# Kernel tuning notes

Hardware: AMD Instinct MI355X
Metric: run time of the kernel (lower is better)

## Reference

```python
import jax, jax.numpy as jnp
import numpy as np

H, D, HID, DIN = 2, 32, 64, 128
NQ, NA, NK = 100000, 200000, 200000
E_KQ, E_QK, E_QA, E_AQ = 800000, 800000, 400000, 400000
EP, EN = 100000, 100000


def setup_inputs() -> dict:
    key = jax.random.key(0)
    ks = jax.random.split(key, 32)
    f = lambda i, shape, s=0.05: jax.random.normal(ks[i], shape, dtype=jnp.float32) * s
    ri = lambda i, n, hi: jax.random.randint(ks[i], (n,), 0, hi)
    return {
        'xq': f(0, (NQ, DIN), 1.0), 'xa': f(1, (NA, DIN), 1.0), 'xk': f(2, (NK, DIN), 1.0),
        'lin_w': f(3, (3, DIN, HID)), 'lin_b': f(4, (3, HID)),
        'k_w': f(5, (3, HID, HID)), 'k_b': f(6, (3, HID)),
        'q_w': f(7, (3, HID, HID)), 'q_b': f(8, (3, HID)),
        'v_w': f(9, (3, HID, HID)), 'v_b': f(10, (3, HID)),
        'a_w': f(11, (3, HID, HID)), 'a_b': f(12, (3, HID)),
        'a_rel': f(13, (4, H, D, D), 0.2), 'm_rel': f(14, (4, H, D, D), 0.2),
        'p_rel': jnp.ones((4, H), dtype=jnp.float32),  # PyG init: ones
        'skip': jnp.ones((3,), dtype=jnp.float32),     # PyG init: ones
        'ei_kq_src': ri(15, E_KQ, NK), 'ei_kq_dst': ri(16, E_KQ, NQ),
        'ei_qk_src': ri(17, E_QK, NQ), 'ei_qk_dst': ri(18, E_QK, NA * 0 + NK),
        'ei_qa_src': ri(19, E_QA, NQ), 'ei_qa_dst': ri(20, E_QA, NA),
        'ei_aq_src': ri(21, E_AQ, NA), 'ei_aq_dst': ri(22, E_AQ, NQ),
        'pos_src': ri(23, EP, NQ), 'pos_dst': ri(24, EP, NA),
        'neg_src': ri(25, EN, NQ), 'neg_dst': ri(26, EN, NA),
    }


def _seg_softmax(alpha, dst, n):
    # softmax over incoming edges per destination node (per head)
    m = jax.ops.segment_max(alpha, dst, num_segments=n)
    m = jnp.where(jnp.isfinite(m), m, 0.0)
    e = jnp.exp(alpha - m[dst])
    s = jax.ops.segment_sum(e, dst, num_segments=n)
    return e / (s[dst] + 1e-16)


def hgt_forward(xq, xa, xk, lin_w, lin_b, k_w, k_b, q_w, q_b, v_w, v_b, a_w, a_b,
                a_rel, m_rel, p_rel, skip, edges):
    # node types: 0=question, 1=answer, 2=knowledge
    xs = [jax.nn.relu(x @ lin_w[i] + lin_b[i]) for i, x in enumerate([xq, xa, xk])]
    ns = [x.shape[0] for x in xs]
    k = [(x @ k_w[i] + k_b[i]).reshape(-1, H, D) for i, x in enumerate(xs)]
    q = [(x @ q_w[i] + q_b[i]).reshape(-1, H, D) for i, x in enumerate(xs)]
    v = [(x @ v_w[i] + v_b[i]).reshape(-1, H, D) for i, x in enumerate(xs)]
    out = [jnp.zeros((n, H, D), dtype=xs[0].dtype) for n in ns]
    scale = 1.0 / jnp.sqrt(jnp.float32(D))
    for st, dt, r, es, ed in edges:
        # per-edge-type head-wise key/value transforms (applied at node level)
        k_rel = jnp.einsum('nhd,hde->nhe', k[st], a_rel[r])
        v_rel = jnp.einsum('nhd,hde->nhe', v[st], m_rel[r])
        alpha = (q[dt][ed] * k_rel[es]).sum(-1) * p_rel[r] * scale  # [E,H]
        a = _seg_softmax(alpha, ed, ns[dt])
        msg = a[:, :, None] * v_rel[es]  # [E,H,D]
        out[dt] = out[dt] + jax.ops.segment_sum(msg, ed, num_segments=ns[dt])
    z = []
    for i in range(3):
        o = jax.nn.gelu(out[i].reshape(-1, H * D), approximate=False) @ a_w[i] + a_b[i]
        beta = jax.nn.sigmoid(skip[i])
        z.append(beta * o + (1.0 - beta) * xs[i])
    return z  # [z_question, z_answer, z_knowledge]; note: HGT.forward never applies self.lin


def reference(xq, xa, xk, lin_w, lin_b, k_w, k_b, q_w, q_b, v_w, v_b, a_w, a_b,
              a_rel, m_rel, p_rel, skip,
              ei_kq_src, ei_kq_dst, ei_qk_src, ei_qk_dst, ei_qa_src, ei_qa_dst,
              ei_aq_src, ei_aq_dst, pos_src, pos_dst, neg_src, neg_dst):
    edges = [
        (2, 0, 0, ei_kq_src, ei_kq_dst),  # knowledge -> question
        (0, 2, 1, ei_qk_src, ei_qk_dst),  # question -> knowledge
        (0, 1, 2, ei_qa_src, ei_qa_dst),  # question -> answer
        (1, 0, 3, ei_aq_src, ei_aq_dst),  # answer -> question
    ]
    zq, za, zk = hgt_forward(xq, xa, xk, lin_w, lin_b, k_w, k_b, q_w, q_b, v_w, v_b,
                             a_w, a_b, a_rel, m_rel, p_rel, skip, edges)
    pos_pred = jax.nn.sigmoid((zq[pos_src] * za[pos_dst]).sum(-1))
    neg_pred = jax.nn.sigmoid((zq[neg_src] * za[neg_dst]).sum(-1))
    return (pos_pred, neg_pred, zq, za, zk)
```

## Files before the change

kernel.cpp:

```cpp
#include <hip/hip_runtime.h>
#include <math.h>

namespace {

constexpr int NQn = 100000, NAn = 200000, NKn = 200000;
constexpr int EPc = 100000, ENc = 100000;
constexpr int ETOT = 2400000, NSEG = 600000;

constexpr long XSB_OFF  = 0;
constexpr long OUTB_OFF = 16000000;
constexpr long QBF_OFF  = 32000000;
constexpr long KV_OFF   = 48000000;
constexpr long ZB_OFF   = 86500000;
constexpr long WTB_OFF  = 96200000;
constexpr long WFB_OFF  = 96250000;
constexpr long INT_OFF  = 96300000;
constexpr long DEG_I  = 0;
constexpr long CUR_I  = 600000;
constexpr long OFFS_I = 1200000;
constexpr long PART_I = 1800064;
constexpr long CSRC_I = 1801088;

constexpr int LINT_U = 0;
constexpr int QT_U   = 24576;
constexpr int AT_U   = 36864;
constexpr int WFT_U  = 49152;

__constant__ long c_rbase[4] = {0, 200000, 300032, 400064};

typedef __attribute__((ext_vector_type(8))) short bf16x8;
typedef __attribute__((ext_vector_type(4))) float f32x4;

__device__ inline f32x4 mfma16(bf16x8 a, bf16x8 b, f32x4 c) {
    return __builtin_amdgcn_mfma_f32_16x16x32_bf16(a, b, c, 0, 0, 0);
}

__device__ inline float gelu_f(float x) {
    return 0.5f * x * (1.0f + erff(x * 0.7071067811865475f));
}
__device__ inline float bf2f(unsigned short u) {
    return __uint_as_float(((unsigned)u) << 16);
}
__device__ inline unsigned short f2bf(float f) {
    unsigned u = __float_as_uint(f);
    return (unsigned short)((u + 0x7fffu + ((u >> 16) & 1u)) >> 16);
}

__device__ inline void type_of_block128(int b, int& t, int& n0) {
    if (b < 782)       { t = 0; n0 = b * 128; }
    else if (b < 2345) { t = 1; n0 = (b - 782) * 128; }
    else               { t = 2; n0 = (b - 2345) * 128; }
}

template<int K>
__device__ inline void stage_bf16(unsigned short* lds, const unsigned short* src,
                                  int n0, int n, int tid)
{
    constexpr int CPR = K / 8;
    for (int c = tid; c < 128 * CPR; c += 256) {
        int row = c / CPR, kc = c % CPR;
        int node = n0 + row; if (node > n - 1) node = n - 1;
        uint4 v = *(const uint4*)&src[(long)node * K + kc * 8];
        int byte = (row * K + kc * 8) * 2;
        *(uint4*)((char*)lds + (byte ^ ((row & 7) << 4))) = v;
    }
}

__device__ inline void stage_out_gelu(unsigned short* lds, const unsigned short* src,
                                      int n0, int n, int tid)
{
    for (int c = tid; c < 128 * 8; c += 256) {
        int row = c >> 3, kc = c & 7;
        int node = n0 + row; if (node > n - 1) node = n - 1;
        uint4 v = *(const uint4*)&src[(long)node * 64 + kc * 8];
        float f0 = gelu_f(bf2f((unsigned short)(v.x & 0xffffu)));
        float f1 = gelu_f(bf2f((unsigned short)(v.x >> 16)));
        float f2 = gelu_f(bf2f((unsigned short)(v.y & 0xffffu)));
        float f3 = gelu_f(bf2f((unsigned short)(v.y >> 16)));
        float f4 = gelu_f(bf2f((unsigned short)(v.z & 0xffffu)));
        float f5 = gelu_f(bf2f((unsigned short)(v.z >> 16)));
        float f6 = gelu_f(bf2f((unsigned short)(v.w & 0xffffu)));
        float f7 = gelu_f(bf2f((unsigned short)(v.w >> 16)));
        uint4 o;
        o.x = (unsigned)f2bf(f0) | ((unsigned)f2bf(f1) << 16);
        o.y = (unsigned)f2bf(f2) | ((unsigned)f2bf(f3) << 16);
        o.z = (unsigned)f2bf(f4) | ((unsigned)f2bf(f5) << 16);
        o.w = (unsigned)f2bf(f6) | ((unsigned)f2bf(f7) << 16);
        int byte = (row * 64 + kc * 8) * 2;
        *(uint4*)((char*)lds + (byte ^ ((row & 7) << 4))) = o;
    }
}

template<int K>
__device__ inline void stage_f32(unsigned short* lds, const float* src,
                                 int n0, int n, int tid)
{
    constexpr int CPR = K / 8;
    for (int c = tid; c < 128 * CPR; c += 256) {
        int row = c / CPR, kc = c % CPR;
        int node = n0 + row; if (node > n - 1) node = n - 1;
        const float* sp = &src[(long)node * K + kc * 8];
        float4 f0 = *(const float4*)sp, f1 = *(const float4*)(sp + 4);
        uint4 v;
        v.x = (unsigned)f2bf(f0.x) | ((unsigned)f2bf(f0.y) << 16);
        v.y = (unsigned)f2bf(f0.z) | ((unsigned)f2bf(f0.w) << 16);
        v.z = (unsigned)f2bf(f1.x) | ((unsigned)f2bf(f1.y) << 16);
        v.w = (unsigned)f2bf(f1.z) | ((unsigned)f2bf(f1.w) << 16);
        int byte = (row * K + kc * 8) * 2;
        *(uint4*)((char*)lds + (byte ^ ((row & 7) << 4))) = v;
    }
}

template<int N, int K>
__device__ inline void stage_w(unsigned short* lds, const unsigned short* wt, int tid)
{
    constexpr int CPR = K / 8;
    for (int c = tid; c < N * CPR; c += 256) {
        int nr = c / CPR, kc = c % CPR;
        uint4 v = *(const uint4*)&wt[nr * K + kc * 8];
        int byte = (nr * K + kc * 8) * 2;
        *(uint4*)((char*)lds + (byte ^ ((nr & 7) << 4))) = v;
    }
}

template<int K, int NF>
__device__ inline void mfma_coreT(const unsigned short* ldsX, const unsigned short* ldsW,
                                  f32x4 (&acc)[2][NF], int lane, int w)
{
    const int lrow = lane & 15, lk = (lane >> 4) * 8;
    #pragma unroll
    for (int ks = 0; ks < K / 32; ++ks) {
        bf16x8 a[2], b[NF];
        #pragma unroll
        for (int mf = 0; mf < 2; ++mf) {
            int row = w * 32 + mf * 16 + lrow;
            int byte = (row * K + ks * 32 + lk) * 2;
            a[mf] = *(const bf16x8*)((const char*)ldsX + (byte ^ ((row & 7) << 4)));
        }
        #pragma unroll
        for (int nf = 0; nf < NF; ++nf) {
            int nr = nf * 16 + lrow;
            int byte = (nr * K + ks * 32 + lk) * 2;
            b[nf] = *(const bf16x8*)((const char*)ldsW + (byte ^ ((nr & 7) << 4)));
        }
        #pragma unroll
        for (int mf = 0; mf < 2; ++mf)
            #pragma unroll
            for (int nf = 0; nf < NF; ++nf)
                acc[mf][nf] = mfma16(b[nf], a[mf], acc[mf][nf]);
    }
}

__global__ void prep_w(const float* __restrict__ lin_w, const float* __restrict__ q_w,
                       const float* __restrict__ a_w, unsigned short* __restrict__ wtb)
{
    int i = blockIdx.x * 256 + threadIdx.x;
    if (i < 24576) {
        int t = i / 8192, rem = i % 8192, nn = rem >> 7, kk = rem & 127;
        wtb[LINT_U + i] = f2bf(lin_w[t * 8192 + kk * 64 + nn]);
    } else if (i < 36864) {
        int j = i - 24576;
        int t = j / 4096, rem = j % 4096, nn = rem >> 6, kk = rem & 63;
        wtb[QT_U + j] = f2bf(q_w[t * 4096 + kk * 64 + nn]);
    } else if (i < 49152) {
        int j = i - 36864;
        int t = j / 4096, rem = j % 4096, nn = rem >> 6, kk = rem & 63;
        wtb[AT_U + j] = f2bf(a_w[t * 4096 + kk * 64 + nn]);
    }
}

__global__ void fuse_weights(const float* __restrict__ kw, const float* __restrict__ kb,
                             const float* __restrict__ vw, const float* __restrict__ vb,
                             const float* __restrict__ a_rel, const float* __restrict__ m_rel,
                             unsigned short* __restrict__ wtb, float* __restrict__ wfb)
{
    const int r = blockIdx.x;
    const int st_tab[4] = {2, 0, 0, 1};
    const int st = st_tab[r];
    const int tid = threadIdx.x;
    for (int idx = tid; idx < 8192; idx += 256) {
        int d = idx >> 7, c = idx & 127;
        int i = c >> 1, which = c & 1;
        int h = i >> 5, e = i & 31;
        const float* w   = (which ? vw : kw) + st * 4096;
        const float* rel = (which ? m_rel : a_rel) + r * 2048;
        float s = 0.f;
        #pragma unroll
        for (int c32 = 0; c32 < 32; ++c32)
            s += w[d * 64 + h * 32 + c32] * rel[h * 1024 + c32 * 32 + e];
        wtb[WFT_U + r * 8192 + c * 64 + d] = f2bf(s);
    }
    for (int idx = tid; idx < 128; idx += 256) {
        int i = idx >> 1, which = idx & 1;
        int h = i >> 5, e = i & 31;
        const float* b   = (which ? vb : kb) + st * 64;
        const float* rel = (which ? m_rel : a_rel) + r * 2048;
        float s = 0.f;
        #pragma unroll
        for (int c32 = 0; c32 < 32; ++c32)
            s += b[h * 32 + c32] * rel[h * 1024 + c32 * 32 + e];
        wfb[r * 128 + idx] = s;
    }
}

__global__ void __launch_bounds__(256)
lin_mfma(const float* __restrict__ xq, const float* __restrict__ xa,
         const float* __restrict__ xk, const unsigned short* __restrict__ wtb,
         const float* __restrict__ lin_b, unsigned short* __restrict__ xsb)
{
    __shared__ unsigned short ldsX[128 * 128];
    __shared__ unsigned short ldsW[64 * 128];
    int t, n0; type_of_block128(blockIdx.x, t, n0);
    const int cnt[3] = {NQn, NAn, NKn};
    const long noff[3] = {0, NQn, NQn + NAn};
    const float* X = (t == 0) ? xq : (t == 1) ? xa : xk;
    const int n = cnt[t];
    const int tid = threadIdx.x;

    stage_w<64, 128>(ldsW, wtb + LINT_U + t * 8192, tid);
    stage_f32<128>(ldsX, X, n0, n, tid);
    __syncthreads();

    const int w = tid >> 6, lane = tid & 63;
    f32x4 acc[2][4] = {};
    mfma_coreT<128, 4>(ldsX, ldsW, acc, lane, w);

    const int nodeL = lane & 15, colG = (lane >> 4) * 4;
    #pragma unroll
    for (int mf = 0; mf < 2; ++mf) {
        int node = n0 + w * 32 + mf * 16 + nodeL;
        if (node < n) {
            #pragma unroll
            for (int nf = 0; nf < 4; ++nf) {
                int col0 = nf * 16 + colG;
                float4 bv = *(const float4*)&lin_b[t * 64 + col0];
                ushort4 o;
                o.x = f2bf(fmaxf(acc[mf][nf][0] + bv.x, 0.f));
                o.y = f2bf(fmaxf(acc[mf][nf][1] + bv.y, 0.f));
                o.z = f2bf(fmaxf(acc[mf][nf][2] + bv.z, 0.f));
                o.w = f2bf(fmaxf(acc[mf][nf][3] + bv.w, 0.f));
                *(ushort4*)&xsb[(noff[t] + node) * 64 + col0] = o;
            }
        }
    }
}

__global__ void __launch_bounds__(256)
qkv_mfma(const unsigned short* __restrict__ xsb, const unsigned short* __restrict__ wtb,
         const float* __restrict__ q_b, const float* __restrict__ wfb,
         unsigned short* __restrict__ qbf, unsigned short* __restrict__ kvb)
{
    __shared__ unsigned short ldsX[128 * 64];
    __shared__ unsigned short ldsW[128 * 64];
    int t, n0; type_of_block128(blockIdx.x, t, n0);
    const int cnt[3] = {NQn, NAn, NKn};
    const long noff[3] = {0, NQn, NQn + NAn};
    const int n = cnt[t];
    const int tid = threadIdx.x;
    const int relA_tab[3] = {1, 3, 0};
    const int rA = relA_tab[t];
    const int nrel = (t == 0) ? 2 : 1;

    stage_bf16<64>(ldsX, xsb + noff[t] * 64, n0, n, tid);
    stage_w<64, 64>(ldsW, wtb + QT_U + t * 4096, tid);
    __syncthreads();

    const int w = tid >> 6, lane = tid & 63;
    const int nodeL = lane & 15, colG = (lane >> 4) * 4;

    {
        f32x4 acc[2][4] = {};
        mfma_coreT<64, 4>(ldsX, ldsW, acc, lane, w);
        #pragma unroll
        for (int mf = 0; mf < 2; ++mf) {
            int node = n0 + w * 32 + mf * 16 + nodeL;
            if (node < n) {
                #pragma unroll
                for (int nf = 0; nf < 4; ++nf) {
                    int col0 = nf * 16 + colG;
                    float4 bv = *(const float4*)&q_b[t * 64 + col0];
                    ushort4 o;
                    o.x = f2bf(acc[mf][nf][0] + bv.x);
                    o.y = f2bf(acc[mf][nf][1] + bv.y);
                    o.z = f2bf(acc[mf][nf][2] + bv.z);
                    o.w = f2bf(acc[mf][nf][3] + bv.w);
                    *(ushort4*)&qbf[(noff[t] + node) * 64 + col0] = o;
                }
            }
        }
    }
    for (int ri = 0; ri < nrel; ++ri) {
        const int r = (ri == 0) ? rA : 2;
        const long rb = c_rbase[r];
        __syncthreads();
        stage_w<128, 64>(ldsW, wtb + WFT_U + r * 8192, tid);
        __syncthreads();
        f32x4 acc[2][8] = {};
        mfma_coreT<64, 8>(ldsX, ldsW, acc, lane, w);
        #pragma unroll
        for (int mf = 0; mf < 2; ++mf) {
            int node = n0 + w * 32 + mf * 16 + nodeL;
            if (node < n) {
                #pragma unroll
                for (int nf = 0; nf < 8; ++nf) {
                    int col0 = nf * 16 + colG;
                    float4 bv = *(const float4*)&wfb[r * 128 + col0];
                    ushort4 o;
                    o.x = f2bf(acc[mf][nf][0] + bv.x);
                    o.y = f2bf(acc[mf][nf][1] + bv.y);
                    o.z = f2bf(acc[mf][nf][2] + bv.z);
                    o.w = f2bf(acc[mf][nf][3] + bv.w);
                    *(ushort4*)&kvb[(rb + node) * 128 + col0] = o;
                }
            }
        }
    }
}

__global__ void __launch_bounds__(256)
head_mfma(const unsigned short* __restrict__ outb, const unsigned short* __restrict__ xsb,
          const unsigned short* __restrict__ wtb, const float* __restrict__ a_b,
          const float* __restrict__ skip, float* __restrict__ z,
          unsigned short* __restrict__ zb)
{
    __shared__ unsigned short ldsX[128 * 64];
    __shared__ unsigned short ldsW[64 * 64];
    int t, n0; type_of_block128(blockIdx.x, t, n0);
    const int cnt[3] = {NQn, NAn, NKn};
    const long noff[3] = {0, NQn, NQn + NAn};
    const long zoff[3] = {200000L, 6600000L, 19400000L};
    const int n = cnt[t];
    const int tid = threadIdx.x;

    stage_w<64, 64>(ldsW, wtb + AT_U + t * 4096, tid);
    stage_out_gelu(ldsX, outb + noff[t] * 64, n0, n, tid);
    __syncthreads();

    const int w = tid >> 6, lane = tid & 63;
    f32x4 acc[2][4] = {};
    mfma_coreT<64, 4>(ldsX, ldsW, acc, lane, w);

    const float beta = 1.f / (1.f + expf(-skip[t]));
    const int nodeL = lane & 15, colG = (lane >> 4) * 4;
    #pragma unroll
    for (int mf = 0; mf < 2; ++mf) {
        int node = n0 + w * 32 + mf * 16 + nodeL;
        if (node < n) {
            #pragma unroll
            for (int nf = 0; nf < 4; ++nf) {
                int col0 = nf * 16 + colG;
                float4 bv = *(const float4*)&a_b[t * 64 + col0];
                ushort4 rv = *(const ushort4*)&xsb[(noff[t] + node) * 64 + col0];
                float4 o;
                o.x = beta * (acc[mf][nf][0] + bv.x) + (1.f - beta) * bf2f(rv.x);
                o.y = beta * (acc[mf][nf][1] + bv.y) + (1.f - beta) * bf2f(rv.y);
                o.z = beta * (acc[mf][nf][2] + bv.z) + (1.f - beta) * bf2f(rv.z);
                o.w = beta * (acc[mf][nf][3] + bv.w) + (1.f - beta) * bf2f(rv.w);
                *(float4*)&z[zoff[t] + (long)node * 64 + col0] = o;
                if (t < 2) {
                    ushort4 p;
                    p.x = f2bf(o.x); p.y = f2bf(o.y); p.z = f2bf(o.z); p.w = f2bf(o.w);
                    long zrow = (t == 0) ? (long)node : 100000L + node;
                    *(ushort4*)&zb[zrow * 64 + col0] = p;
                }
            }
        }
    }
}

__global__ void csr_count_all(const int* __restrict__ d0, const int* __restrict__ d1,
                              const int* __restrict__ d2, const int* __restrict__ d3,
                              int* __restrict__ deg)
{
    int gid = blockIdx.x * 256 + threadIdx.x;
    if (gid < 800000)       atomicAdd(&deg[d0[gid]], 1);
    else if (gid < 1600000) atomicAdd(&deg[100000 + d1[gid - 800000]], 1);
    else if (gid < 2000000) atomicAdd(&deg[300000 + d2[gid - 1600000]], 1);
    else if (gid < 2400000) atomicAdd(&deg[500000 + d3[gid - 2000000]], 1);
}

__global__ void csr_fill_all(const int* __restrict__ s0, const int* __restrict__ d0,
                             const int* __restrict__ s1, const int* __restrict__ d1,
                             const int* __restrict__ s2, const int* __restrict__ d2,
                             const int* __restrict__ s3, const int* __restrict__ d3,
                             const int* __restrict__ off, int* __restrict__ cur,
                             int* __restrict__ csrc)
{
    int gid = blockIdx.x * 256 + threadIdx.x;
    int seg, s;
    if (gid < 800000)       { seg = d0[gid];                    s = s0[gid]; }
    else if (gid < 1600000) { seg = 100000 + d1[gid - 800000];  s = s1[gid - 800000]; }
    else if (gid < 2000000) { seg = 300000 + d2[gid - 1600000]; s = s2[gid - 1600000]; }
    else if (gid < 2400000) { seg = 500000 + d3[gid - 2000000]; s = s3[gid - 2000000]; }
    else return;
    int slot = off[seg] + atomicAdd(&cur[seg], 1);
    csrc[slot] = s;
}

__global__ void scan1(const int* __restrict__ in, int* __restrict__ out,
                      int* __restrict__ part, int n)
{
    __shared__ int lds[256];
    const int tid = threadIdx.x;
    const int base = blockIdx.x * 1024 + tid * 4;
    int v[4];
    #pragma unroll
    for (int k = 0; k < 4; ++k) v[k] = (base + k < n) ? in[base + k] : 0;
    int tsum = v[0] + v[1] + v[2] + v[3];
    lds[tid] = tsum;
    __syncthreads();
    for (int off = 1; off < 256; off <<= 1) {
        int t = (tid >= off) ? lds[tid - off] : 0;
        __syncthreads();
        lds[tid] += t;
        __syncthreads();
    }
    int excl = lds[tid] - tsum;
    #pragma unroll
    for (int k = 0; k < 4; ++k) {
        if (base + k < n) out[base + k] = excl;
        excl += v[k];
    }
    if (tid == 255) part[blockIdx.x] = lds[255];
}

__global__ void scan2(int* __restrict__ part, int nb)
{
    __shared__ int lds[256];
    const int tid = threadIdx.x;
    const int base = tid * 4;
    int v[4];
    #pragma unroll
    for (int k = 0; k < 4; ++k) v[k] = (base + k < nb) ? part[base + k] : 0;
    int tsum = v[0] + v[1] + v[2] + v[3];
    lds[tid] = tsum;
    __syncthreads();
    for (int off = 1; off < 256; off <<= 1) {
        int t = (tid >= off) ? lds[tid - off] : 0;
        __syncthreads();
        lds[tid] += t;
        __syncthreads();
    }
    int excl = lds[tid] - tsum;
    #pragma unroll
    for (int k = 0; k < 4; ++k) {
        if (base + k < nb) part[base + k] = excl;
        excl += v[k];
    }
}

__global__ void scan3(int* __restrict__ off, const int* __restrict__ part, int n, int E)
{
    int i = blockIdx.x * 256 + threadIdx.x;
    if (i < n) off[i] += part[i >> 10];
    if (i == 0) off[n] = E;
}

__device__ inline void attn_node(const int* __restrict__ csrc, int begin, int end,
                                 const unsigned short* __restrict__ kvt,
                                 const float qv[4], int j, float res[4])
{
    float ss = 0.f, a0 = 0.f, a1 = 0.f, a2 = 0.f, a3 = 0.f;

    for (int t = begin; t < end; t += 2) {
        bool vB = (t + 1 < end);
        int sA = csrc[t];
        int sB = csrc[vB ? t + 1 : t];
        uint4 kA = *(const uint4*)(kvt + (long)sA * 128 + j * 8);
        uint4 kB = *(const uint4*)(kvt + (long)sB * 128 + j * 8);

        float ka0 = __uint_as_float(kA.x << 16), va0 = __uint_as_float(kA.x & 0xffff0000u);
        float ka1 = __uint_as_float(kA.y << 16), va1 = __uint_as_float(kA.y & 0xffff0000u);
        float ka2 = __uint_as_float(kA.z << 16), va2 = __uint_as_float(kA.z & 0xffff0000u);
        float ka3 = __uint_as_float(kA.w << 16), va3 = __uint_as_float(kA.w & 0xffff0000u);
        float kb0 = __uint_as_float(kB.x << 16), vb0 = __uint_as_float(kB.x & 0xffff0000u);
        float kb1 = __uint_as_float(kB.y << 16), vb1 = __uint_as_float(kB.y & 0xffff0000u);
        float kb2 = __uint_as_float(kB.z << 16), vb2 = __uint_as_float(kB.z & 0xffff0000u);
        float kb3 = __uint_as_float(kB.w << 16), vb3 = __uint_as_float(kB.w & 0xffff0000u);

        float pA = ka0 * qv[0] + ka1 * qv[1] + ka2 * qv[2] + ka3 * qv[3];
        float pB = kb0 * qv[0] + kb1 * qv[1] + kb2 * qv[2] + kb3 * qv[3];
        pA += __shfl_xor(pA, 1);  pB += __shfl_xor(pB, 1);
        pA += __shfl_xor(pA, 2);  pB += __shfl_xor(pB, 2);
        pA += __shfl_xor(pA, 4);  pB += __shfl_xor(pB, 4);

        float wA = exp2f(fminf(pA, 115.f));
        float wB = vB ? exp2f(fminf(pB, 115.f)) : 0.f;

        ss += wA + wB;
        a0 += wA * va0 + wB * vb0;
        a1 += wA * va1 + wB * vb1;
        a2 += wA * va2 + wB * vb2;
        a3 += wA * va3 + wB * vb3;
    }

    float inv = 1.f / (ss + 1e-16f);
    res[0] = a0 * inv; res[1] = a1 * inv; res[2] = a2 * inv; res[3] = a3 * inv;
}

__global__ void __launch_bounds__(256)
attn_all(const int* __restrict__ off, const int* __restrict__ csrc,
         const unsigned short* __restrict__ qbf, const unsigned short* __restrict__ kv,
         const float* __restrict__ prel, float scale, unsigned short* __restrict__ outb)
{
    const int tid = threadIdx.x;
    const int nid = blockIdx.x * 16 + (tid >> 4);
    const int j = tid & 15;
    const int h = j >> 3;
    const float l2e = 1.4426950408889634f;

    long row; int segA, segB = -1; long kbA, kbB = 0; float psA, psB = 0.f;
    if (nid < 100000) {
        row = nid;
        segA = nid;            kbA = c_rbase[0]; psA = prel[0 + h] * scale * l2e;
        segB = 500000 + nid;   kbB = c_rbase[3]; psB = prel[6 + h] * scale * l2e;
    } else if (nid < 300000) {
        int kk = nid - 100000;
        row = 300000 + kk;
        segA = 100000 + kk;    kbA = c_rbase[1]; psA = prel[2 + h] * scale * l2e;
    } else {
        int aa = nid - 300000;
        row = 100000 + aa;
        segA = 300000 + aa;    kbA = c_rbase[2]; psA = prel[4 + h] * scale * l2e;
    }

    ushort4 q4 = *(const ushort4*)&qbf[row * 64 + 4 * j];
    float qraw[4] = {bf2f(q4.x), bf2f(q4.y), bf2f(q4.z), bf2f(q4.w)};

    float res[4];
    {
        float qv[4] = {qraw[0] * psA, qraw[1] * psA, qraw[2] * psA, qraw[3] * psA};
        attn_node(csrc, off[segA], off[segA + 1], kv + kbA * 128, qv, j, res);
    }
    if (segB >= 0) {
        float qv[4] = {qraw[0] * psB, qraw[1] * psB, qraw[2] * psB, qraw[3] * psB};
        float r2[4];
        attn_node(csrc, off[segB], off[segB + 1], kv + kbB * 128, qv, j, r2);
        res[0] += r2[0]; res[1] += r2[1]; res[2] += r2[2]; res[3] += r2[3];
    }

    ushort4 o;
    o.x = f2bf(res[0]); o.y = f2bf(res[1]); o.z = f2bf(res[2]); o.w = f2bf(res[3]);
    *(ushort4*)&outb[row * 64 + 4 * j] = o;
}

__global__ void pred_all(const int* __restrict__ psrc, const int* __restrict__ pdst,
                         const int* __restrict__ nsrc, const int* __restrict__ ndst,
                         const unsigned short* __restrict__ zb, float* __restrict__ out)
{
    int t = blockIdx.x * 256 + threadIdx.x;
    int g = t >> 3, lane = t & 7;
    if (g >= EPc + ENc) return;
    int s, d;
    if (g < EPc) { s = psrc[g]; d = pdst[g]; }
    else         { int gg = g - EPc; s = nsrc[gg]; d = ndst[gg]; }
    uint4 zs = *(const uint4*)&zb[(long)s * 64 + lane * 8];
    uint4 zd = *(const uint4*)&zb[(100000L + d) * 64 + lane * 8];
    float p = 0.f;
    p += bf2f((unsigned short)(zs.x & 0xffffu)) * bf2f((unsigned short)(zd.x & 0xffffu));
    p += bf2f((unsigned short)(zs.x >> 16))     * bf2f((unsigned short)(zd.x >> 16));
    p += bf2f((unsigned short)(zs.y & 0xffffu)) * bf2f((unsigned short)(zd.y & 0xffffu));
    p += bf2f((unsigned short)(zs.y >> 16))     * bf2f((unsigned short)(zd.y >> 16));
    p += bf2f((unsigned short)(zs.z & 0xffffu)) * bf2f((unsigned short)(zd.z & 0xffffu));
    p += bf2f((unsigned short)(zs.z >> 16))     * bf2f((unsigned short)(zd.z >> 16));
    p += bf2f((unsigned short)(zs.w & 0xffffu)) * bf2f((unsigned short)(zd.w & 0xffffu));
    p += bf2f((unsigned short)(zs.w >> 16))     * bf2f((unsigned short)(zd.w >> 16));
    p += __shfl_xor(p, 1);
    p += __shfl_xor(p, 2);
    p += __shfl_xor(p, 4);
    if (lane == 0) out[g] = 1.f / (1.f + expf(-p));
}

}

extern "C" void kernel_launch(void* const* d_in, const int* in_sizes, int n_in,
                              void* d_out, int out_size, void* d_ws, size_t ws_size,
                              hipStream_t stream)
{
    const float* xq    = (const float*)d_in[0];
    const float* xa    = (const float*)d_in[1];
    const float* xk    = (const float*)d_in[2];
    const float* lin_w = (const float*)d_in[3];
    const float* lin_b = (const float*)d_in[4];
    const float* k_w   = (const float*)d_in[5];
    const float* k_b   = (const float*)d_in[6];
    const float* q_w   = (const float*)d_in[7];
    const float* q_b   = (const float*)d_in[8];
    const float* v_w   = (const float*)d_in[9];
    const float* v_b   = (const float*)d_in[10];
    const float* a_w   = (const float*)d_in[11];
    const float* a_b   = (const float*)d_in[12];
    const float* a_rel = (const float*)d_in[13];
    const float* m_rel = (const float*)d_in[14];
    const float* p_rel = (const float*)d_in[15];
    const float* skip  = (const float*)d_in[16];
    const int* esrc[4] = {(const int*)d_in[17], (const int*)d_in[19], (const int*)d_in[21], (const int*)d_in[23]};
    const int* edst[4] = {(const int*)d_in[18], (const int*)d_in[20], (const int*)d_in[22], (const int*)d_in[24]};
    const int* pos_src = (const int*)d_in[25];
    const int* pos_dst = (const int*)d_in[26];
    const int* neg_src = (const int*)d_in[27];
    const int* neg_dst = (const int*)d_in[28];

    float* ws   = (float*)d_ws;
    float* outp = (float*)d_out;
    int*   wi   = (int*)(ws + INT_OFF);
    unsigned short* xsb  = (unsigned short*)(ws + XSB_OFF);
    unsigned short* outb = (unsigned short*)(ws + OUTB_OFF);
    unsigned short* qbf  = (unsigned short*)(ws + QBF_OFF);
    unsigned short* kvb  = (unsigned short*)(ws + KV_OFF);
    unsigned short* zbb  = (unsigned short*)(ws + ZB_OFF);
    unsigned short* wtb  = (unsigned short*)(ws + WTB_OFF);
    float*          wfb  = ws + WFB_OFF;

    hipMemsetAsync(wi + DEG_I, 0, 1200000L * sizeof(int), stream);
    csr_count_all<<<(ETOT + 255) / 256, 256, 0, stream>>>(
        edst[0], edst[1], edst[2], edst[3], wi + DEG_I);
    const int nb = (NSEG + 1023) / 1024;
    scan1<<<nb, 256, 0, stream>>>(wi + DEG_I, wi + OFFS_I, wi + PART_I, NSEG);
    scan2<<<1, 256, 0, stream>>>(wi + PART_I, nb);
    scan3<<<(NSEG + 255) / 256, 256, 0, stream>>>(wi + OFFS_I, wi + PART_I, NSEG, ETOT);
    csr_fill_all<<<(ETOT + 255) / 256, 256, 0, stream>>>(
        esrc[0], edst[0], esrc[1], edst[1], esrc[2], edst[2], esrc[3], edst[3],
        wi + OFFS_I, wi + CUR_I, wi + CSRC_I);

    fuse_weights<<<4, 256, 0, stream>>>(k_w, k_b, v_w, v_b, a_rel, m_rel, wtb, wfb);
    prep_w<<<192, 256, 0, stream>>>(lin_w, q_w, a_w, wtb);

    lin_mfma<<<3908, 256, 0, stream>>>(xq, xa, xk, wtb, lin_b, xsb);
    qkv_mfma<<<3908, 256, 0, stream>>>(xsb, wtb, q_b, wfb, qbf, kvb);

    const float scale = 0.17677669529663687f;
    attn_all<<<31250, 256, 0, stream>>>(wi + OFFS_I, wi + CSRC_I, qbf, kvb,
                                        p_rel, scale, outb);

    head_mfma<<<3908, 256, 0, stream>>>(outb, xsb, wtb, a_b, skip, outp, zbb);

    pred_all<<<(200000 * 8 + 255) / 256, 256, 0, stream>>>(
        pos_src, pos_dst, neg_src, neg_dst, zbb, outp);
}
```

Before: 653.1 us.

## Fuse input projection with QKV projection and merge weight prep kernels

The input linear+ReLU projection and the Q/K/V projection now run in one kernel. The projected features stay in LDS for the second GEMM instead of being re-read from global memory, though xsb is still written because the head stage needs it. The two weight-preparation kernels are merged into one launch. The attention inner loop now processes four edges per iteration instead of two to raise memory-level parallelism, at the cost of more registers.

Result: faster. 636.1 us (-2.6%).

```diff
diff --git a/kernel.cpp b/kernel.cpp
--- a/kernel.cpp
+++ b/kernel.cpp
@@ -50,20 +50,6 @@
     if (b < 782)       { t = 0; n0 = b * 128; }
     else if (b < 2345) { t = 1; n0 = (b - 782) * 128; }
     else               { t = 2; n0 = (b - 2345) * 128; }
-}
-
-template<int K>
-__device__ inline void stage_bf16(unsigned short* lds, const unsigned short* src,
-                                  int n0, int n, int tid)
-{
-    constexpr int CPR = K / 8;
-    for (int c = tid; c < 128 * CPR; c += 256) {
-        int row = c / CPR, kc = c % CPR;
-        int node = n0 + row; if (node > n - 1) node = n - 1;
-        uint4 v = *(const uint4*)&src[(long)node * K + kc * 8];
-        int byte = (row * K + kc * 8) * 2;
-        *(uint4*)((char*)lds + (byte ^ ((row & 7) << 4))) = v;
-    }
 }
 
 __device__ inline void stage_out_gelu(unsigned short* lds, const unsigned short* src,
@@ -151,126 +137,112 @@
     }
 }
 
-__global__ void prep_w(const float* __restrict__ lin_w, const float* __restrict__ q_w,
-                       const float* __restrict__ a_w, unsigned short* __restrict__ wtb)
-{
-    int i = blockIdx.x * 256 + threadIdx.x;
-    if (i < 24576) {
-        int t = i / 8192, rem = i % 8192, nn = rem >> 7, kk = rem & 127;
-        wtb[LINT_U + i] = f2bf(lin_w[t * 8192 + kk * 64 + nn]);
-    } else if (i < 36864) {
-        int j = i - 24576;
-        int t = j / 4096, rem = j % 4096, nn = rem >> 6, kk = rem & 63;
-        wtb[QT_U + j] = f2bf(q_w[t * 4096 + kk * 64 + nn]);
-    } else if (i < 49152) {
-        int j = i - 36864;
-        int t = j / 4096, rem = j % 4096, nn = rem >> 6, kk = rem & 63;
-        wtb[AT_U + j] = f2bf(a_w[t * 4096 + kk * 64 + nn]);
-    }
-}
-
-__global__ void fuse_weights(const float* __restrict__ kw, const float* __restrict__ kb,
-                             const float* __restrict__ vw, const float* __restrict__ vb,
-                             const float* __restrict__ a_rel, const float* __restrict__ m_rel,
-                             unsigned short* __restrict__ wtb, float* __restrict__ wfb)
-{
-    const int r = blockIdx.x;
-    const int st_tab[4] = {2, 0, 0, 1};
-    const int st = st_tab[r];
+__global__ void prep_all(const float* __restrict__ lin_w, const float* __restrict__ q_w,
+                         const float* __restrict__ a_w,
+                         const float* __restrict__ kw, const float* __restrict__ kb,
+                         const float* __restrict__ vw, const float* __restrict__ vb,
+                         const float* __restrict__ a_rel, const float* __restrict__ m_rel,
+                         unsigned short* __restrict__ wtb, float* __restrict__ wfb)
+{
     const int tid = threadIdx.x;
-    for (int idx = tid; idx < 8192; idx += 256) {
-        int d = idx >> 7, c = idx & 127;
-        int i = c >> 1, which = c & 1;
-        int h = i >> 5, e = i & 31;
-        const float* w   = (which ? vw : kw) + st * 4096;
-        const float* rel = (which ? m_rel : a_rel) + r * 2048;
-        float s = 0.f;
-        #pragma unroll
-        for (int c32 = 0; c32 < 32; ++c32)
-            s += w[d * 64 + h * 32 + c32] * rel[h * 1024 + c32 * 32 + e];
-        wtb[WFT_U + r * 8192 + c * 64 + d] = f2bf(s);
-    }
-    for (int idx = tid; idx < 128; idx += 256) {
-        int i = idx >> 1, which = idx & 1;
-        int h = i >> 5, e = i & 31;
-        const float* b   = (which ? vb : kb) + st * 64;
-        const float* rel = (which ? m_rel : a_rel) + r * 2048;
-        float s = 0.f;
-        #pragma unroll
-        for (int c32 = 0; c32 < 32; ++c32)
-            s += b[h * 32 + c32] * rel[h * 1024 + c32 * 32 + e];
-        wfb[r * 128 + idx] = s;
+    if (blockIdx.x < 4) {
+        const int r = blockIdx.x;
+        const int st_tab[4] = {2, 0, 0, 1};
+        const int st = st_tab[r];
+        for (int idx = tid; idx < 8192; idx += 256) {
+            int d = idx >> 7, c = idx & 127;
+            int i = c >> 1, which = c & 1;
+            int h = i >> 5, e = i & 31;
+            const float* w   = (which ? vw : kw) + st * 4096;
+            const float* rel = (which ? m_rel : a_rel) + r * 2048;
+            float s = 0.f;
+            #pragma unroll
+            for (int c32 = 0; c32 < 32; ++c32)
+                s += w[d * 64 + h * 32 + c32] * rel[h * 1024 + c32 * 32 + e];
+            wtb[WFT_U + r * 8192 + c * 64 + d] = f2bf(s);
+        }
+        for (int idx = tid; idx < 128; idx += 256) {
+            int i = idx >> 1, which = idx & 1;
+            int h = i >> 5, e = i & 31;
+            const float* b   = (which ? vb : kb) + st * 64;
+            const float* rel = (which ? m_rel : a_rel) + r * 2048;
+            float s = 0.f;
+            #pragma unroll
+            for (int c32 = 0; c32 < 32; ++c32)
+                s += b[h * 32 + c32] * rel[h * 1024 + c32 * 32 + e];
+            wfb[r * 128 + idx] = s;
+        }
+    } else {
+        int i = (blockIdx.x - 4) * 256 + tid;
+        if (i < 24576) {
+            int t = i / 8192, rem = i % 8192, nn = rem >> 7, kk = rem & 127;
+            wtb[LINT_U + i] = f2bf(lin_w[t * 8192 + kk * 64 + nn]);
+        } else if (i < 36864) {
+            int j = i - 24576;
+            int t = j / 4096, rem = j % 4096, nn = rem >> 6, kk = rem & 63;
+            wtb[QT_U + j] = f2bf(q_w[t * 4096 + kk * 64 + nn]);
+        } else if (i < 49152) {
+            int j = i - 36864;
+            int t = j / 4096, rem = j % 4096, nn = rem >> 6, kk = rem & 63;
+            wtb[AT_U + j] = f2bf(a_w[t * 4096 + kk * 64 + nn]);
+        }
     }
 }
 
 __global__ void __launch_bounds__(256)
-lin_mfma(const float* __restrict__ xq, const float* __restrict__ xa,
-         const float* __restrict__ xk, const unsigned short* __restrict__ wtb,
-         const float* __restrict__ lin_b, unsigned short* __restrict__ xsb)
+linqkv_mfma(const float* __restrict__ xq, const float* __restrict__ xa,
+            const float* __restrict__ xk, const unsigned short* __restrict__ wtb,
+            const float* __restrict__ lin_b, const float* __restrict__ q_b,
+            const float* __restrict__ wfb, unsigned short* __restrict__ xsb,
+            unsigned short* __restrict__ qbf, unsigned short* __restrict__ kvb)
 {
     __shared__ unsigned short ldsX[128 * 128];
-    __shared__ unsigned short ldsW[64 * 128];
+    __shared__ unsigned short ldsXS[128 * 64];
     int t, n0; type_of_block128(blockIdx.x, t, n0);
     const int cnt[3] = {NQn, NAn, NKn};
     const long noff[3] = {0, NQn, NQn + NAn};
     const float* X = (t == 0) ? xq : (t == 1) ? xa : xk;
     const int n = cnt[t];
     const int tid = threadIdx.x;
-
-    stage_w<64, 128>(ldsW, wtb + LINT_U + t * 8192, tid);
-    stage_f32<128>(ldsX, X, n0, n, tid);
-    __syncthreads();
-
     const int w = tid >> 6, lane = tid & 63;
-    f32x4 acc[2][4] = {};
-    mfma_coreT<128, 4>(ldsX, ldsW, acc, lane, w);
-
     const int nodeL = lane & 15, colG = (lane >> 4) * 4;
-    #pragma unroll
-    for (int mf = 0; mf < 2; ++mf) {
-        int node = n0 + w * 32 + mf * 16 + nodeL;
-        if (node < n) {
-            #pragma unroll
-            for (int nf = 0; nf < 4; ++nf) {
-                int col0 = nf * 16 + colG;
-                float4 bv = *(const float4*)&lin_b[t * 64 + col0];
-                ushort4 o;
-                o.x = f2bf(fmaxf(acc[mf][nf][0] + bv.x, 0.f));
-                o.y = f2bf(fmaxf(acc[mf][nf][1] + bv.y, 0.f));
-                o.z = f2bf(fmaxf(acc[mf][nf][2] + bv.z, 0.f));
-                o.w = f2bf(fmaxf(acc[mf][nf][3] + bv.w, 0.f));
-                *(ushort4*)&xsb[(noff[t] + node) * 64 + col0] = o;
-            }
-        }
-    }
-}
-
-__global__ void __launch_bounds__(256)
-qkv_mfma(const unsigned short* __restrict__ xsb, const unsigned short* __restrict__ wtb,
-         const float* __restrict__ q_b, const float* __restrict__ wfb,
-         unsigned short* __restrict__ qbf, unsigned short* __restrict__ kvb)
-{
-    __shared__ unsigned short ldsX[128 * 64];
-    __shared__ unsigned short ldsW[128 * 64];
-    int t, n0; type_of_block128(blockIdx.x, t, n0);
-    const int cnt[3] = {NQn, NAn, NKn};
-    const long noff[3] = {0, NQn, NQn + NAn};
-    const int n = cnt[t];
-    const int tid = threadIdx.x;
     const int relA_tab[3] = {1, 3, 0};
     const int rA = relA_tab[t];
     const int nrel = (t == 0) ? 2 : 1;
 
-    stage_bf16<64>(ldsX, xsb + noff[t] * 64, n0, n, tid);
-    stage_w<64, 64>(ldsW, wtb + QT_U + t * 4096, tid);
+    stage_w<64, 128>(ldsXS, wtb + LINT_U + t * 8192, tid);
+    stage_f32<128>(ldsX, X, n0, n, tid);
     __syncthreads();
 
-    const int w = tid >> 6, lane = tid & 63;
-    const int nodeL = lane & 15, colG = (lane >> 4) * 4;
+    f32x4 acc[2][4] = {};
+    mfma_coreT<128, 4>(ldsX, ldsXS, acc, lane, w);
+    __syncthreads();
+
+    #pragma unroll
+    for (int mf = 0; mf < 2; ++mf) {
+        int nl = w * 32 + mf * 16 + nodeL;
+        int node = n0 + nl;
+        #pragma unroll
+        for (int nf = 0; nf < 4; ++nf) {
+            int col0 = nf * 16 + colG;
+            float4 bv = *(const float4*)&lin_b[t * 64 + col0];
+            ushort4 o;
+            o.x = f2bf(fmaxf(acc[mf][nf][0] + bv.x, 0.f));
+            o.y = f2bf(fmaxf(acc[mf][nf][1] + bv.y, 0.f));
+            o.z = f2bf(fmaxf(acc[mf][nf][2] + bv.z, 0.f));
+            o.w = f2bf(fmaxf(acc[mf][nf][3] + bv.w, 0.f));
+            int byte = (nl * 64 + col0) * 2;
+            *(ushort4*)((char*)ldsXS + (byte ^ ((nl & 7) << 4))) = o;
+            if (node < n)
+                *(ushort4*)&xsb[(noff[t] + node) * 64 + col0] = o;
+        }
+    }
+    stage_w<64, 64>(ldsX, wtb + QT_U + t * 4096, tid);
+    __syncthreads();
 
     {
-        f32x4 acc[2][4] = {};
-        mfma_coreT<64, 4>(ldsX, ldsW, acc, lane, w);
+        f32x4 qa[2][4] = {};
+        mfma_coreT<64, 4>(ldsXS, ldsX, qa, lane, w);
         #pragma unroll
         for (int mf = 0; mf < 2; ++mf) {
             int node = n0 + w * 32 + mf * 16 + nodeL;
@@ -280,23 +252,24 @@
                     int col0 = nf * 16 + colG;
                     float4 bv = *(const float4*)&q_b[t * 64 + col0];
                     ushort4 o;
-                    o.x = f2bf(acc[mf][nf][0] + bv.x);
-                    o.y = f2bf(acc[mf][nf][1] + bv.y);
-                    o.z = f2bf(acc[mf][nf][2] + bv.z);
-                    o.w = f2bf(acc[mf][nf][3] + bv.w);
+                    o.x = f2bf(qa[mf][nf][0] + bv.x);
+                    o.y = f2bf(qa[mf][nf][1] + bv.y);
+                    o.z = f2bf(qa[mf][nf][2] + bv.z);
+                    o.w = f2bf(qa[mf][nf][3] + bv.w);
                     *(ushort4*)&qbf[(noff[t] + node) * 64 + col0] = o;
                 }
             }
         }
     }
+
     for (int ri = 0; ri < nrel; ++ri) {
         const int r = (ri == 0) ? rA : 2;
         const long rb = c_rbase[r];
         __syncthreads();
-        stage_w<128, 64>(ldsW, wtb + WFT_U + r * 8192, tid);
+        stage_w<128, 64>(ldsX, wtb + WFT_U + r * 8192, tid);
         __syncthreads();
-        f32x4 acc[2][8] = {};
-        mfma_coreT<64, 8>(ldsX, ldsW, acc, lane, w);
+        f32x4 ka[2][8] = {};
+        mfma_coreT<64, 8>(ldsXS, ldsX, ka, lane, w);
         #pragma unroll
         for (int mf = 0; mf < 2; ++mf) {
             int node = n0 + w * 32 + mf * 16 + nodeL;
@@ -306,10 +279,10 @@
                     int col0 = nf * 16 + colG;
                     float4 bv = *(const float4*)&wfb[r * 128 + col0];
                     ushort4 o;
-                    o.x = f2bf(acc[mf][nf][0] + bv.x);
-                    o.y = f2bf(acc[mf][nf][1] + bv.y);
-                    o.z = f2bf(acc[mf][nf][2] + bv.z);
-                    o.w = f2bf(acc[mf][nf][3] + bv.w);
+                    o.x = f2bf(ka[mf][nf][0] + bv.x);
+                    o.y = f2bf(ka[mf][nf][1] + bv.y);
+                    o.z = f2bf(ka[mf][nf][2] + bv.z);
+                    o.w = f2bf(ka[mf][nf][3] + bv.w);
                     *(ushort4*)&kvb[(rb + node) * 128 + col0] = o;
                 }
             }
@@ -462,36 +435,47 @@
 {
     float ss = 0.f, a0 = 0.f, a1 = 0.f, a2 = 0.f, a3 = 0.f;
 
-    for (int t = begin; t < end; t += 2) {
-        bool vB = (t + 1 < end);
-        int sA = csrc[t];
-        int sB = csrc[vB ? t + 1 : t];
-        uint4 kA = *(const uint4*)(kvt + (long)sA * 128 + j * 8);
-        uint4 kB = *(const uint4*)(kvt + (long)sB * 128 + j * 8);
-
-        float ka0 = __uint_as_float(kA.x << 16), va0 = __uint_as_float(kA.x & 0xffff0000u);
-        float ka1 = __uint_as_float(kA.y << 16), va1 = __uint_as_float(kA.y & 0xffff0000u);
-        float ka2 = __uint_as_float(kA.z << 16), va2 = __uint_as_float(kA.z & 0xffff0000u);
-        float ka3 = __uint_as_float(kA.w << 16), va3 = __uint_as_float(kA.w & 0xffff0000u);
-        float kb0 = __uint_as_float(kB.x << 16), vb0 = __uint_as_float(kB.x & 0xffff0000u);
-        float kb1 = __uint_as_float(kB.y << 16), vb1 = __uint_as_float(kB.y & 0xffff0000u);
-        float kb2 = __uint_as_float(kB.z << 16), vb2 = __uint_as_float(kB.z & 0xffff0000u);
-        float kb3 = __uint_as_float(kB.w << 16), vb3 = __uint_as_float(kB.w & 0xffff0000u);
-
-        float pA = ka0 * qv[0] + ka1 * qv[1] + ka2 * qv[2] + ka3 * qv[3];
-        float pB = kb0 * qv[0] + kb1 * qv[1] + kb2 * qv[2] + kb3 * qv[3];
-        pA += __shfl_xor(pA, 1);  pB += __shfl_xor(pB, 1);
-        pA += __shfl_xor(pA, 2);  pB += __shfl_xor(pB, 2);
-        pA += __shfl_xor(pA, 4);  pB += __shfl_xor(pB, 4);
-
-        float wA = exp2f(fminf(pA, 115.f));
-        float wB = vB ? exp2f(fminf(pB, 115.f)) : 0.f;
-
-        ss += wA + wB;
-        a0 += wA * va0 + wB * vb0;
-        a1 += wA * va1 + wB * vb1;
-        a2 += wA * va2 + wB * vb2;
-        a3 += wA * va3 + wB * vb3;
+    for (int t = begin; t < end; t += 4) {
+        bool v1 = (t + 1 < end), v2 = (t + 2 < end), v3 = (t + 3 < end);
+        int s0 = csrc[t];
+        int s1 = csrc[v1 ? t + 1 : t];
+        int s2 = csrc[v2 ? t + 2 : t];
+        int s3 = csrc[v3 ? t + 3 : t];
+        uint4 k0 = *(const uint4*)(kvt + (long)s0 * 128 + j * 8);
+        uint4 k1 = *(const uint4*)(kvt + (long)s1 * 128 + j * 8);
+        uint4 k2 = *(const uint4*)(kvt + (long)s2 * 128 + j * 8);
+        uint4 k3 = *(const uint4*)(kvt + (long)s3 * 128 + j * 8);
+
+        float p0 = __uint_as_float(k0.x << 16) * qv[0] + __uint_as_float(k0.y << 16) * qv[1]
+                 + __uint_as_float(k0.z << 16) * qv[2] + __uint_as_float(k0.w << 16) * qv[3];
+        float p1 = __uint_as_float(k1.x << 16) * qv[0] + __uint_as_float(k1.y << 16) * qv[1]
+                 + __uint_as_float(k1.z << 16) * qv[2] + __uint_as_float(k1.w << 16) * qv[3];
+        float p2 = __uint_as_float(k2.x << 16) * qv[0] + __uint_as_float(k2.y << 16) * qv[1]
+                 + __uint_as_float(k2.z << 16) * qv[2] + __uint_as_float(k2.w << 16) * qv[3];
+        float p3 = __uint_as_float(k3.x << 16) * qv[0] + __uint_as_float(k3.y << 16) * qv[1]
+                 + __uint_as_float(k3.z << 16) * qv[2] + __uint_as_float(k3.w << 16) * qv[3];
+
+        p0 += __shfl_xor(p0, 1);  p1 += __shfl_xor(p1, 1);
+        p2 += __shfl_xor(p2, 1);  p3 += __shfl_xor(p3, 1);
+        p0 += __shfl_xor(p0, 2);  p1 += __shfl_xor(p1, 2);
+        p2 += __shfl_xor(p2, 2);  p3 += __shfl_xor(p3, 2);
+        p0 += __shfl_xor(p0, 4);  p1 += __shfl_xor(p1, 4);
+        p2 += __shfl_xor(p2, 4);  p3 += __shfl_xor(p3, 4);
+
+        float w0 = exp2f(fminf(p0, 115.f));
+        float w1 = v1 ? exp2f(fminf(p1, 115.f)) : 0.f;
+        float w2 = v2 ? exp2f(fminf(p2, 115.f)) : 0.f;
+        float w3 = v3 ? exp2f(fminf(p3, 115.f)) : 0.f;
+
+        ss += (w0 + w1) + (w2 + w3);
+        a0 += w0 * __uint_as_float(k0.x & 0xffff0000u) + w1 * __uint_as_float(k1.x & 0xffff0000u)
+            + w2 * __uint_as_float(k2.x & 0xffff0000u) + w3 * __uint_as_float(k3.x & 0xffff0000u);
+        a1 += w0 * __uint_as_float(k0.y & 0xffff0000u) + w1 * __uint_as_float(k1.y & 0xffff0000u)
+            + w2 * __uint_as_float(k2.y & 0xffff0000u) + w3 * __uint_as_float(k3.y & 0xffff0000u);
+        a2 += w0 * __uint_as_float(k0.z & 0xffff0000u) + w1 * __uint_as_float(k1.z & 0xffff0000u)
+            + w2 * __uint_as_float(k2.z & 0xffff0000u) + w3 * __uint_as_float(k3.z & 0xffff0000u);
+        a3 += w0 * __uint_as_float(k0.w & 0xffff0000u) + w1 * __uint_as_float(k1.w & 0xffff0000u)
+            + w2 * __uint_as_float(k2.w & 0xffff0000u) + w3 * __uint_as_float(k3.w & 0xffff0000u);
     }
 
     float inv = 1.f / (ss + 1e-16f);
@@ -623,11 +607,11 @@
         esrc[0], edst[0], esrc[1], edst[1], esrc[2], edst[2], esrc[3], edst[3],
         wi + OFFS_I, wi + CUR_I, wi + CSRC_I);
 
-    fuse_weights<<<4, 256, 0, stream>>>(k_w, k_b, v_w, v_b, a_rel, m_rel, wtb, wfb);
-    prep_w<<<192, 256, 0, stream>>>(lin_w, q_w, a_w, wtb);
-
-    lin_mfma<<<3908, 256, 0, stream>>>(xq, xa, xk, wtb, lin_b, xsb);
-    qkv_mfma<<<3908, 256, 0, stream>>>(xsb, wtb, q_b, wfb, qbf, kvb);
+    prep_all<<<196, 256, 0, stream>>>(lin_w, q_w, a_w, k_w, k_b, v_w, v_b,
+                                      a_rel, m_rel, wtb, wfb);
+
+    linqkv_mfma<<<3908, 256, 0, stream>>>(xq, xa, xk, wtb, lin_b, q_b, wfb,
+                                          xsb, qbf, kvb);
 
     const float scale = 0.17677669529663687f;
     attn_all<<<31250, 256, 0, stream>>>(wi + OFFS_I, wi + CSRC_I, qbf, kvb,
```
